# Kernel optimization log

Hardware: AMD Instinct MI355X
Metric: run time of the kernel (lower is better)

Reference implementation:

```python
import jax, jax.numpy as jnp
import numpy as np

N = 8192          # points per cloud
IN_C = 256        # in_channels
OUT_C = 256       # out_channels
SC = IN_C // 4    # shortcut_out_channels
KNN = 32          # neighbors gathered per point
KP = 15           # kernel points (standard KPConv)
RADIUS = 0.12
EXTENT = RADIUS * 2.0 / 2.5   # radius * kp_extent / conv_radius
NEG_SLOPE = 0.1
EPS = 1e-5


def setup_inputs() -> dict:
    key = jax.random.key(0)
    ks = jax.random.split(key, 10)
    src = jax.random.normal(ks[0], (N, IN_C), jnp.float32)
    tgt = jax.random.normal(ks[1], (N, IN_C), jnp.float32)
    src_coords = jax.random.uniform(ks[2], (N, 3), jnp.float32)
    tgt_coords = jax.random.uniform(ks[3], (N, 3), jnp.float32)
    W_in = jax.random.normal(ks[4], (IN_C, SC), jnp.float32) / np.sqrt(IN_C)
    b_in = jnp.zeros((SC,), jnp.float32)
    kernel_pts = jax.random.normal(ks[5], (KP, 3), jnp.float32) * (0.7 * EXTENT)
    W_kp = jax.random.normal(ks[6], (KP, SC, SC), jnp.float32) / np.sqrt(KP * SC)
    W_out = jax.random.normal(ks[7], (SC, OUT_C), jnp.float32) / np.sqrt(SC)
    b_out = jnp.zeros((OUT_C,), jnp.float32)
    gamma = jnp.ones((OUT_C,), jnp.float32)
    beta = jnp.zeros((OUT_C,), jnp.float32)
    return dict(src=src, tgt=tgt, src_coords=src_coords, tgt_coords=tgt_coords,
                W_in=W_in, b_in=b_in, kernel_pts=kernel_pts, W_kp=W_kp,
                W_out=W_out, b_out=b_out, gamma=gamma, beta=beta)


def _one_cloud(x, coords, W_in, b_in, kernel_pts, W_kp, W_out, b_out, gamma, beta):
    # 1x1 conv in: [N, IN_C] -> [N, SC]
    h = x @ W_in + b_in

    # neighbor search: kNN by squared distance, masked to the conv radius
    d2 = jnp.sum((coords[:, None, :] - coords[None, :, :]) ** 2, axis=-1)  # [N, N]
    _, idx = jax.lax.top_k(-d2, KNN)                                       # [N, KNN]
    nb_coords = coords[idx]                                                # [N, KNN, 3]
    rel = nb_coords - coords[:, None, :]                                   # [N, KNN, 3]
    in_range = jnp.sum(rel ** 2, axis=-1) <= RADIUS ** 2                   # [N, KNN]

    # KPConv: linear correlation to kernel points, masked neighbor aggregate
    diff = rel[:, :, None, :] - kernel_pts[None, None, :, :]               # [N, KNN, KP, 3]
    dist = jnp.sqrt(jnp.sum(diff ** 2, axis=-1))                           # [N, KNN, KP]
    infl = jnp.maximum(1.0 - dist / EXTENT, 0.0) * in_range[:, :, None]    # [N, KNN, KP]
    nb_feats = h[idx]                                                      # [N, KNN, SC]
    agg = jnp.einsum('nkp,nkc->npc', infl, nb_feats)                       # [N, KP, SC]
    h = jnp.einsum('npc,pcd->nd', agg, W_kp)                               # [N, SC]

    # 1x1 conv out: [N, SC] -> [N, OUT_C]
    y = h @ W_out + b_out

    # batch norm over points (training-mode statistics) + affine
    mu = jnp.mean(y, axis=0)
    var = jnp.mean((y - mu) ** 2, axis=0)
    y = gamma * (y - mu) * jax.lax.rsqrt(var + EPS) + beta

    # leaky relu
    return jnp.where(y > 0, y, NEG_SLOPE * y)


def reference(src, tgt, src_coords, tgt_coords, W_in, b_in, kernel_pts, W_kp,
              W_out, b_out, gamma, beta):
    params = (W_in, b_in, kernel_pts, W_kp, W_out, b_out, gamma, beta)
    s = _one_cloud(src, src_coords, *params)
    t = _one_cloud(tgt, tgt_coords, *params)
    return (s, t, src_coords, tgt_coords)
```

## Files before the change

### kernel.cpp

```cpp
#include <hip/hip_runtime.h>
#include <stdint.h>

#define NPTS 8192
#define KNN 32
#define KPN 15
#define SCC 64
#define OUTC 256
#define R2F 0.0144f
#define INV_EXT (1.0f/0.096f)
#define SCAP 128
#define NT 8
#define COB 32
#define GD 8
#define NCELL (GD*GD*GD)
#define KJ (KPN*SCC)
#define AGP 968

typedef float  f32x4  __attribute__((ext_vector_type(4)));
typedef __bf16 bf16x8 __attribute__((ext_vector_type(8)));
typedef __bf16 bf16x4 __attribute__((ext_vector_type(4)));

__device__ __forceinline__ int cell_of(float x) {
  int c = (int)(x * (float)GD);
  return c < 0 ? 0 : (c > GD-1 ? GD-1 : c);
}

__global__ __launch_bounds__(256) void prep_k(
    const float* __restrict__ scd, const float* __restrict__ tcd,
    float* __restrict__ out,
    const float* __restrict__ Wkp, __bf16* __restrict__ WkpT,
    const float* __restrict__ Win, __bf16* __restrict__ WinF)
{
  int b = blockIdx.x, t = threadIdx.x;
  if (b < 192) {
    int i = b*256 + t;
    out[i] = (i < NPTS*3) ? scd[i] : tcd[i - NPTS*3];
  } else if (b < 432) {
    int i = (b - 192)*256 + t;
    int j = i >> 6, d = i & 63;
    WkpT[(size_t)d*KJ + j] = (__bf16)Wkp[i];
  } else {
    int i = (b - 432)*256 + t;
    int j = i & 7, lane = (i >> 3) & 63, cc = i >> 9;
    int kc = cc >> 2, ct = cc & 3;
    int g16 = lane >> 4, p = lane & 15;
    int k = kc*32 + g16*8 + j;
    WinF[i] = (__bf16)Win[(size_t)k*64 + ct*16 + p];
  }
}

__global__ __launch_bounds__(1024) void grid_build(
    const float* __restrict__ cA, const float* __restrict__ cB,
    unsigned int* __restrict__ starts,
    unsigned int* __restrict__ cursor,
    float* __restrict__ stats)
{
  __shared__ unsigned int hcnt[2][NCELL];
  __shared__ unsigned int a[NCELL], b[NCELL];
  int t = threadIdx.x;
  if (t < NCELL) { hcnt[0][t] = 0u; hcnt[1][t] = 0u; }
  stats[t] = 0.f;
  __syncthreads();
  for (int i = t; i < 2*NPTS; i += 1024) {
    int cloud = i >> 13, n = i & 8191;
    const float* coords = cloud ? cB : cA;
    int cx = cell_of(coords[(size_t)n*3]);
    int cy = cell_of(coords[(size_t)n*3+1]);
    int cz = cell_of(coords[(size_t)n*3+2]);
    atomicAdd(&hcnt[cloud][(cz*GD + cy)*GD + cx], 1u);
  }
  __syncthreads();
  for (int cloud = 0; cloud < 2; ++cloud) {
    if (t < NCELL) a[t] = hcnt[cloud][t];
    __syncthreads();
    unsigned int *s = a, *d = b;
    for (int off = 1; off < NCELL; off <<= 1) {
      if (t < NCELL) {
        unsigned int x = s[t];
        if (t >= off) x += s[t - off];
        d[t] = x;
      }
      __syncthreads();
      unsigned int* tmp = s; s = d; d = tmp;
    }
    if (t < NCELL) {
      unsigned int inc = s[t];
      unsigned int exc = inc - hcnt[cloud][t];
      starts[cloud*520 + t] = exc;
      cursor[cloud*NCELL + t] = exc;
      if (t == NCELL-1) starts[cloud*520 + NCELL] = inc;
    }
    __syncthreads();
  }
}

__global__ __launch_bounds__(256) void grid_scatter(
    const float* __restrict__ cA, const float* __restrict__ cB,
    unsigned int* __restrict__ cursor, float4* __restrict__ sorted,
    float4* __restrict__ coords4)
{
  int i = blockIdx.x*256 + threadIdx.x;
  int cloud = i >> 13, n = i & 8191;
  const float* coords = cloud ? cB : cA;
  float x = coords[(size_t)n*3], y = coords[(size_t)n*3+1], z = coords[(size_t)n*3+2];
  coords4[(size_t)cloud*NPTS + n] = make_float4(x, y, z, 0.f);
  int cell = (cell_of(z)*GD + cell_of(y))*GD + cell_of(x);
  unsigned int slot = atomicAdd(&cursor[cloud*NCELL + cell], 1u);
  sorted[(size_t)cloud*NPTS + slot] = make_float4(x, y, z, __int_as_float(n));
}

__global__ __launch_bounds__(256) void knn_convin_k(
    const float4* __restrict__ coords4,
    const unsigned int* __restrict__ starts, const float4* __restrict__ sorted,
    short* __restrict__ fidx,
    const float* __restrict__ src, const float* __restrict__ tgt,
    const __bf16* __restrict__ WinF, const float* __restrict__ bin,
    __bf16* __restrict__ h)
{
  __shared__ unsigned long long surv[4][SCAP];
  int bId = blockIdx.x;
  int t = threadIdx.x, w = t >> 6, lane = t & 63;
  if (bId < 256) {
    int rt = bId*4 + w;
    int row0 = rt*16;
    const float* x = (row0 >> 13) ? tgt : src;
    int n0 = row0 & 8191;
    int g16 = lane >> 4, p = lane & 15;
    const float* xrow = x + (size_t)(n0 + p)*256;
    f32x4 acc[4];
    #pragma unroll
    for (int ct = 0; ct < 4; ++ct) {
      float bb = bin[ct*16 + p];
      acc[ct] = (f32x4){bb, bb, bb, bb};
    }
    #pragma unroll
    for (int kc = 0; kc < 8; ++kc) {
      float4 xa = *(const float4*)(xrow + kc*32 + g16*8);
      float4 xb = *(const float4*)(xrow + kc*32 + g16*8 + 4);
      bf16x8 af;
      af[0]=(__bf16)xa.x; af[1]=(__bf16)xa.y; af[2]=(__bf16)xa.z; af[3]=(__bf16)xa.w;
      af[4]=(__bf16)xb.x; af[5]=(__bf16)xb.y; af[6]=(__bf16)xb.z; af[7]=(__bf16)xb.w;
      #pragma unroll
      for (int ct = 0; ct < 4; ++ct) {
        bf16x8 bf = *(const bf16x8*)(WinF + (size_t)(kc*4 + ct)*512 + lane*8);
        acc[ct] = __builtin_amdgcn_mfma_f32_16x16x32_bf16(af, bf, acc[ct], 0,0,0);
      }
    }
    #pragma unroll
    for (int r = 0; r < 4; ++r) {
      bf16x4 o;
      o[0] = (__bf16)acc[0][r]; o[1] = (__bf16)acc[1][r];
      o[2] = (__bf16)acc[2][r]; o[3] = (__bf16)acc[3][r];
      *(bf16x4*)(h + (size_t)(row0 + g16*4 + r)*SCC + p*4) = o;
    }
    return;
  }
  int q = (bId - 256)*4 + w;
  int cloud = q >> 13, n = q & 8191;
  float4 qc = coords4[(size_t)cloud*NPTS + n];
  float qx = qc.x, qy = qc.y, qz = qc.z;
  int cx = cell_of(qx), cy = cell_of(qy), cz = cell_of(qz);
  const unsigned int* st = starts + cloud*520;
  const float4* sp = sorted + (size_t)cloud*NPTS;
  int c0 = cx > 0 ? cx-1 : 0;
  int c1 = cx < GD-1 ? cx+1 : GD-1;
  unsigned int cnt = 0;
  for (int dz = -1; dz <= 1; ++dz) {
    int zz = cz + dz; if (zz < 0 || zz > GD-1) continue;
    for (int dy = -1; dy <= 1; ++dy) {
      int yy = cy + dy; if (yy < 0 || yy > GD-1) continue;
      int rb = (zz*GD + yy)*GD;
      unsigned int s = st[rb + c0];
      unsigned int e = st[rb + c1 + 1];
      for (unsigned int jj = s; jj < e; jj += 64) {
        unsigned int j = jj + lane;
        bool keep = false; float d2 = 0.f; unsigned int oi = 0;
        if (j < e) {
          float4 p4 = sp[j];
          float dx = qx-p4.x, dyy = qy-p4.y, dzz = qz-p4.z;
          d2 = fmaf(dx, dx, fmaf(dyy, dyy, dzz*dzz));
          oi = __float_as_uint(p4.w);
          keep = (d2 <= R2F);
        }
        unsigned long long m = __ballot(keep);
        if (keep) {
          unsigned int before = __builtin_amdgcn_mbcnt_hi(
              (unsigned int)(m >> 32),
              __builtin_amdgcn_mbcnt_lo((unsigned int)m, 0u));
          unsigned int pos = cnt + before;
          if (pos < SCAP)
            surv[w][pos] = ((unsigned long long)__float_as_uint(d2) << 32) | oi;
        }
        cnt += (unsigned int)__popcll(m);
      }
    }
  }
  int C = (int)cnt; if (C > SCAP) C = SCAP;
  unsigned long long k0 = (lane      < C) ? surv[w][lane]      : ~0ULL;
  unsigned long long k1 = (lane + 64 < C) ? surv[w][lane + 64] : ~0ULL;
  int r0 = 0, r1 = 0;
  for (int j = 0; j < C; ++j) {
    unsigned long long kj = surv[w][j];
    r0 += (kj < k0);
    r1 += (kj < k1);
  }
  size_t g = (size_t)cloud*NPTS + n;
  if (k0 != ~0ULL && r0 < KNN) fidx[g*KNN + r0] = (short)(k0 & 0xffffu);
  if (k1 != ~0ULL && r1 < KNN) fidx[g*KNN + r1] = (short)(k1 & 0xffffu);
  if (lane >= C && lane < KNN) fidx[g*KNN + lane] = (short)-1;
}

__global__ __launch_bounds__(512) void kpconv_fused(
    const float4* __restrict__ coords4,
    const float* __restrict__ kpts, const short* __restrict__ fidx,
    const __bf16* __restrict__ h, const __bf16* __restrict__ WkpT,
    float* __restrict__ h2)
{
  __shared__ __bf16 agg_s[NT][AGP];
  __shared__ float  red2[2*4*16*17];
  int t = threadIdx.x;
  int w = t >> 6, lane = t & 63;
  int gq = blockIdx.x*NT + w;
  int cloud = gq >> 13, n = gq & 8191;
  const float4* c4 = coords4 + (size_t)cloud*NPTS;
  int idxreg = fidx[(size_t)gq*KNN + (lane & 31)];
  float4 qc = c4[n];
  float qx = qc.x, qy = qc.y, qz = qc.z;
  int g16 = lane >> 4;
  int p   = lane & 15;
  int pc  = p < KPN ? p : 0;
  float kpx = kpts[pc*3], kpy = kpts[pc*3+1], kpz = kpts[pc*3+2];
  bf16x8 afrag;
  int idxs[8];
  #pragma unroll
  for (int j = 0; j < 8; ++j) {
    int k = g16*8 + j;
    int idx = __shfl(idxreg, k);
    idxs[j] = idx < 0 ? 0 : idx;
    float4 nc = c4[idxs[j]];
    float wv = 0.f;
    if (idx >= 0 && p < KPN) {
      float dx = (nc.x - qx) - kpx;
      float dy = (nc.y - qy) - kpy;
      float dz = (nc.z - qz) - kpz;
      float d = sqrtf(fmaf(dx, dx, fmaf(dy, dy, dz*dz)));
      wv = fmaxf(1.0f - d*INV_EXT, 0.0f);
    }
    afrag[j] = (__bf16)wv;
  }
  bf16x8 bfrag0, bfrag1, bfrag2, bfrag3;
  #pragma unroll
  for (int j = 0; j < 8; ++j) {
    bf16x4 hv = *(const bf16x4*)(h + ((size_t)(cloud*NPTS + idxs[j]))*SCC + p*4);
    bfrag0[j] = hv[0];
    bfrag1[j] = hv[1];
    bfrag2[j] = hv[2];
    bfrag3[j] = hv[3];
  }
  f32x4 acc0 = {0.f,0.f,0.f,0.f}, acc1 = acc0, acc2 = acc0, acc3 = acc0;
  acc0 = __builtin_amdgcn_mfma_f32_16x16x32_bf16(afrag, bfrag0, acc0, 0, 0, 0);
  acc1 = __builtin_amdgcn_mfma_f32_16x16x32_bf16(afrag, bfrag1, acc1, 0, 0, 0);
  acc2 = __builtin_amdgcn_mfma_f32_16x16x32_bf16(afrag, bfrag2, acc2, 0, 0, 0);
  acc3 = __builtin_amdgcn_mfma_f32_16x16x32_bf16(afrag, bfrag3, acc3, 0, 0, 0);
  #pragma unroll
  for (int r = 0; r < 4; ++r) {
    int pp = g16*4 + r;
    if (pp < KPN) {
      agg_s[w][pp*SCC +      p] = (__bf16)acc0[r];
      agg_s[w][pp*SCC + 16 + p] = (__bf16)acc1[r];
      agg_s[w][pp*SCC + 32 + p] = (__bf16)acc2[r];
      agg_s[w][pp*SCC + 48 + p] = (__bf16)acc3[r];
    }
  }
  __syncthreads();
  {
    int dt = w & 3, kh = w >> 2;
    int ptb = p & 7;
    const __bf16* arow = WkpT + (size_t)(dt*16 + p)*KJ + kh*480 + g16*8;
    const __bf16* brow = &agg_s[ptb][kh*480 + g16*8];
    f32x4 accB = {0.f,0.f,0.f,0.f};
    #pragma unroll
    for (int s = 0; s < 15; ++s) {
      bf16x8 af = *(const bf16x8*)(arow + s*32);
      bf16x8 bfr = *(const bf16x8*)(brow + s*32);
      accB = __builtin_amdgcn_mfma_f32_16x16x32_bf16(af, bfr, accB, 0, 0, 0);
    }
    if (p < 8) {
      #pragma unroll
      for (int r = 0; r < 4; ++r)
        red2[((kh*4 + dt)*16 + g16*4 + r)*17 + p] = accB[r];
    }
  }
  __syncthreads();
  {
    int pt = t >> 6, d = t & 63;
    float v = red2[d*17 + pt] + red2[(64 + d)*17 + pt];
    h2[((size_t)blockIdx.x*NT + pt)*SCC + d] = v;
  }
}

__global__ __launch_bounds__(512) void conv_out_bn(
    const float* __restrict__ h2, const float* __restrict__ W,
    const float* __restrict__ b, float* __restrict__ y,
    float* __restrict__ stats)
{
  __shared__ float w_s[SCC*OUTC];
  __shared__ float h_s[COB][SCC];
  __shared__ float rs_s[2][OUTC];
  __shared__ float rs2_s[2][OUTC];
  int t = threadIdx.x;
  int d = t & 255, rg = t >> 8;
  int row0 = blockIdx.x*COB;
  int cloud = (int)(blockIdx.x >> 8);
  {
    const float4* gw = (const float4*)W;
    float4* lw = (float4*)w_s;
    #pragma unroll
    for (int i = 0; i < 8; ++i) lw[t + 512*i] = gw[t + 512*i];
    const float4* gh = (const float4*)(h2 + (size_t)row0*SCC);
    ((float4*)h_s)[t] = gh[t];
  }
  __syncthreads();
  float acc[16];
  float bb = b[d];
  #pragma unroll
  for (int r = 0; r < 16; ++r) acc[r] = bb;
  int rb = rg*16;
  #pragma unroll 4
  for (int c4 = 0; c4 < 16; ++c4) {
    float w0 = w_s[(c4*4+0)*OUTC + d];
    float w1 = w_s[(c4*4+1)*OUTC + d];
    float w2 = w_s[(c4*4+2)*OUTC + d];
    float w3 = w_s[(c4*4+3)*OUTC + d];
    #pragma unroll
    for (int r = 0; r < 16; ++r) {
      float4 hv = *(const float4*)&h_s[rb + r][c4*4];
      acc[r] = fmaf(hv.x,w0, fmaf(hv.y,w1, fmaf(hv.z,w2, fmaf(hv.w,w3, acc[r]))));
    }
  }
  float s = 0.f, s2 = 0.f;
  #pragma unroll
  for (int r = 0; r < 16; ++r) {
    float v = acc[r];
    y[((size_t)row0 + rb + r)*OUTC + d] = v;
    s += v; s2 = fmaf(v, v, s2);
  }
  rs_s[rg][d] = s; rs2_s[rg][d] = s2;
  __syncthreads();
  if (rg == 0) {
    atomicAdd(&stats[cloud*512 + d],       s  + rs_s[1][d]);
    atomicAdd(&stats[cloud*512 + 256 + d], s2 + rs2_s[1][d]);
  }
}

__global__ __launch_bounds__(256) void bn_apply_k(
    float* __restrict__ y, const float* __restrict__ stats,
    const float* __restrict__ gamma, const float* __restrict__ beta)
{
  size_t e = (size_t)blockIdx.x*256 + threadIdx.x;
  int c = (int)(e & 255);
  int cloud = (int)(e >> 21);
  float s  = stats[cloud*512 + c];
  float s2 = stats[cloud*512 + 256 + c];
  float mu  = s * (1.0f/NPTS);
  float var = fmaxf(s2 * (1.0f/NPTS) - mu*mu, 0.f);
  float sc = gamma[c] * rsqrtf(var + 1e-5f);
  float sh = beta[c] - mu*sc;
  float v = fmaf(y[e], sc, sh);
  v = v > 0.f ? v : 0.1f*v;
  y[e] = v;
}

extern "C" void kernel_launch(void* const* d_in, const int* in_sizes, int n_in,
                              void* d_out, int out_size, void* d_ws, size_t ws_size,
                              hipStream_t stream)
{
  (void)in_sizes; (void)n_in; (void)out_size; (void)ws_size;
  const float* src   = (const float*)d_in[0];
  const float* tgt   = (const float*)d_in[1];
  const float* scd   = (const float*)d_in[2];
  const float* tcd   = (const float*)d_in[3];
  const float* W_in  = (const float*)d_in[4];
  const float* b_in  = (const float*)d_in[5];
  const float* kpts  = (const float*)d_in[6];
  const float* W_kp  = (const float*)d_in[7];
  const float* W_out = (const float*)d_in[8];
  const float* b_out = (const float*)d_in[9];
  const float* gamma = (const float*)d_in[10];
  const float* beta  = (const float*)d_in[11];

  char* ws = (char*)d_ws;
  __bf16* h    = (__bf16*)ws;
  float* h2    = (float*)(ws + (4u<<20));
  short* fidx  = (short*)(ws + (8u<<20));
  float* stats = (float*)(ws + (9u<<20));
  __bf16* WkpT = (__bf16*)(ws + (9u<<20) + (64u<<10));
  __bf16* WinF = (__bf16*)(ws + (9u<<20) + (256u<<10));
  float4* coords4 = (float4*)(ws + (9u<<20) + (512u<<10));
  unsigned int* starts = (unsigned int*)(ws + (4u<<20) + (8u<<10));
  unsigned int* cursor = (unsigned int*)(ws + (4u<<20) + (16u<<10));
  float4* sorted       = (float4*)(ws + (4u<<20) + (32u<<10));

  float* yout = (float*)d_out;

  prep_k<<<496, 256, 0, stream>>>(scd, tcd, yout + (size_t)2*NPTS*OUTC,
                                  W_kp, WkpT, W_in, WinF);
  grid_build<<<1, 1024, 0, stream>>>(scd, tcd, starts, cursor, stats);
  grid_scatter<<<64, 256, 0, stream>>>(scd, tcd, cursor, sorted, coords4);
  knn_convin_k<<<4352, 256, 0, stream>>>(coords4, starts, sorted, fidx,
                                         src, tgt, WinF, b_in, h);
  kpconv_fused<<<2048, 512, 0, stream>>>(coords4, kpts, fidx, h, WkpT, h2);
  conv_out_bn<<<512, 512, 0, stream>>>(h2, W_out, b_out, yout, stats);
  bn_apply_k<<<16384, 256, 0, stream>>>(yout, stats, gamma, beta);
}
```

Before: 202.9 us.

## Process 16 spatially sorted points per block in KPConv with full-K MFMA

```diff
diff --git a/kernel.cpp b/kernel.cpp
--- a/kernel.cpp
+++ b/kernel.cpp
@@ -9,12 +9,11 @@
 #define R2F 0.0144f
 #define INV_EXT (1.0f/0.096f)
 #define SCAP 128
-#define NT 8
 #define COB 32
 #define GD 8
 #define NCELL (GD*GD*GD)
 #define KJ (KPN*SCC)
-#define AGP 968
+#define AGP2 1000
 
 typedef float  f32x4  __attribute__((ext_vector_type(4)));
 typedef __bf16 bf16x8 __attribute__((ext_vector_type(8)));
@@ -210,92 +209,102 @@
   if (lane >= C && lane < KNN) fidx[g*KNN + lane] = (short)-1;
 }
 
-__global__ __launch_bounds__(512) void kpconv_fused(
-    const float4* __restrict__ coords4,
+__global__ __launch_bounds__(512, 4) void kpconv_fused(
+    const float4* __restrict__ coords4, const float4* __restrict__ sorted,
     const float* __restrict__ kpts, const short* __restrict__ fidx,
     const __bf16* __restrict__ h, const __bf16* __restrict__ WkpT,
     float* __restrict__ h2)
 {
-  __shared__ __bf16 agg_s[NT][AGP];
-  __shared__ float  red2[2*4*16*17];
+  __shared__ __bf16 agg_s[16][AGP2];
+  __shared__ float  red2[4*16*17];
+  __shared__ int    oidx_s[16];
   int t = threadIdx.x;
   int w = t >> 6, lane = t & 63;
-  int gq = blockIdx.x*NT + w;
-  int cloud = gq >> 13, n = gq & 8191;
+  int b = blockIdx.x;
+  int cloud = b >> 9;
+  int sbase = (b & 511)*16;
   const float4* c4 = coords4 + (size_t)cloud*NPTS;
-  int idxreg = fidx[(size_t)gq*KNN + (lane & 31)];
-  float4 qc = c4[n];
-  float qx = qc.x, qy = qc.y, qz = qc.z;
+  const float4* sp = sorted + (size_t)cloud*NPTS;
   int g16 = lane >> 4;
   int p   = lane & 15;
   int pc  = p < KPN ? p : 0;
   float kpx = kpts[pc*3], kpy = kpts[pc*3+1], kpz = kpts[pc*3+2];
-  bf16x8 afrag;
-  int idxs[8];
+  bf16x8 afrag[2];
+  int idxs[2][8];
+  int orig[2];
   #pragma unroll
-  for (int j = 0; j < 8; ++j) {
-    int k = g16*8 + j;
-    int idx = __shfl(idxreg, k);
-    idxs[j] = idx < 0 ? 0 : idx;
-    float4 nc = c4[idxs[j]];
-    float wv = 0.f;
-    if (idx >= 0 && p < KPN) {
-      float dx = (nc.x - qx) - kpx;
-      float dy = (nc.y - qy) - kpy;
-      float dz = (nc.z - qz) - kpz;
-      float d = sqrtf(fmaf(dx, dx, fmaf(dy, dy, dz*dz)));
-      wv = fmaxf(1.0f - d*INV_EXT, 0.0f);
-    }
-    afrag[j] = (__bf16)wv;
-  }
-  bf16x8 bfrag0, bfrag1, bfrag2, bfrag3;
+  for (int hf = 0; hf < 2; ++hf) {
+    int lp = w*2 + hf;
+    float4 se = sp[sbase + lp];
+    int o = (int)__float_as_uint(se.w);
+    orig[hf] = o;
+    if (lane == 0) oidx_s[lp] = o;
+    int idxreg = fidx[((size_t)cloud*NPTS + o)*KNN + (lane & 31)];
+    float qx = se.x, qy = se.y, qz = se.z;
+    #pragma unroll
+    for (int j = 0; j < 8; ++j) {
+      int k = g16*8 + j;
+      int idx = __shfl(idxreg, k);
+      idxs[hf][j] = idx < 0 ? 0 : idx;
+      float4 nc = c4[idxs[hf][j]];
+      float wv = 0.f;
+      if (idx >= 0 && p < KPN) {
+        float dx = (nc.x - qx) - kpx;
+        float dy = (nc.y - qy) - kpy;
+        float dz = (nc.z - qz) - kpz;
+        float d = sqrtf(fmaf(dx, dx, fmaf(dy, dy, dz*dz)));
+        wv = fmaxf(1.0f - d*INV_EXT, 0.0f);
+      }
+      afrag[hf][j] = (__bf16)wv;
+    }
+  }
   #pragma unroll
-  for (int j = 0; j < 8; ++j) {
-    bf16x4 hv = *(const bf16x4*)(h + ((size_t)(cloud*NPTS + idxs[j]))*SCC + p*4);
-    bfrag0[j] = hv[0];
-    bfrag1[j] = hv[1];
-    bfrag2[j] = hv[2];
-    bfrag3[j] = hv[3];
-  }
-  f32x4 acc0 = {0.f,0.f,0.f,0.f}, acc1 = acc0, acc2 = acc0, acc3 = acc0;
-  acc0 = __builtin_amdgcn_mfma_f32_16x16x32_bf16(afrag, bfrag0, acc0, 0, 0, 0);
-  acc1 = __builtin_amdgcn_mfma_f32_16x16x32_bf16(afrag, bfrag1, acc1, 0, 0, 0);
-  acc2 = __builtin_amdgcn_mfma_f32_16x16x32_bf16(afrag, bfrag2, acc2, 0, 0, 0);
-  acc3 = __builtin_amdgcn_mfma_f32_16x16x32_bf16(afrag, bfrag3, acc3, 0, 0, 0);
-  #pragma unroll
-  for (int r = 0; r < 4; ++r) {
-    int pp = g16*4 + r;
-    if (pp < KPN) {
-      agg_s[w][pp*SCC +      p] = (__bf16)acc0[r];
-      agg_s[w][pp*SCC + 16 + p] = (__bf16)acc1[r];
-      agg_s[w][pp*SCC + 32 + p] = (__bf16)acc2[r];
-      agg_s[w][pp*SCC + 48 + p] = (__bf16)acc3[r];
-    }
-  }
-  __syncthreads();
-  {
-    int dt = w & 3, kh = w >> 2;
-    int ptb = p & 7;
-    const __bf16* arow = WkpT + (size_t)(dt*16 + p)*KJ + kh*480 + g16*8;
-    const __bf16* brow = &agg_s[ptb][kh*480 + g16*8];
+  for (int hf = 0; hf < 2; ++hf) {
+    bf16x8 bfrag0, bfrag1, bfrag2, bfrag3;
+    #pragma unroll
+    for (int j = 0; j < 8; ++j) {
+      bf16x4 hv = *(const bf16x4*)(h + ((size_t)cloud*NPTS + idxs[hf][j])*SCC + p*4);
+      bfrag0[j] = hv[0]; bfrag1[j] = hv[1]; bfrag2[j] = hv[2]; bfrag3[j] = hv[3];
+    }
+    f32x4 a0 = {0.f,0.f,0.f,0.f}, a1 = a0, a2 = a0, a3 = a0;
+    a0 = __builtin_amdgcn_mfma_f32_16x16x32_bf16(afrag[hf], bfrag0, a0, 0,0,0);
+    a1 = __builtin_amdgcn_mfma_f32_16x16x32_bf16(afrag[hf], bfrag1, a1, 0,0,0);
+    a2 = __builtin_amdgcn_mfma_f32_16x16x32_bf16(afrag[hf], bfrag2, a2, 0,0,0);
+    a3 = __builtin_amdgcn_mfma_f32_16x16x32_bf16(afrag[hf], bfrag3, a3, 0,0,0);
+    int lp = w*2 + hf;
+    #pragma unroll
+    for (int r = 0; r < 4; ++r) {
+      int pp = g16*4 + r;
+      if (pp < KPN) {
+        agg_s[lp][pp*SCC +      p] = (__bf16)a0[r];
+        agg_s[lp][pp*SCC + 16 + p] = (__bf16)a1[r];
+        agg_s[lp][pp*SCC + 32 + p] = (__bf16)a2[r];
+        agg_s[lp][pp*SCC + 48 + p] = (__bf16)a3[r];
+      }
+    }
+  }
+  __syncthreads();
+  if (w < 4) {
+    int dt = w;
+    const __bf16* arow = WkpT + (size_t)(dt*16 + p)*KJ + g16*8;
+    const __bf16* brow = &agg_s[p][g16*8];
     f32x4 accB = {0.f,0.f,0.f,0.f};
     #pragma unroll
-    for (int s = 0; s < 15; ++s) {
-      bf16x8 af = *(const bf16x8*)(arow + s*32);
+    for (int s = 0; s < 30; ++s) {
+      bf16x8 af  = *(const bf16x8*)(arow + s*32);
       bf16x8 bfr = *(const bf16x8*)(brow + s*32);
       accB = __builtin_amdgcn_mfma_f32_16x16x32_bf16(af, bfr, accB, 0, 0, 0);
     }
-    if (p < 8) {
-      #pragma unroll
-      for (int r = 0; r < 4; ++r)
-        red2[((kh*4 + dt)*16 + g16*4 + r)*17 + p] = accB[r];
-    }
-  }
-  __syncthreads();
-  {
-    int pt = t >> 6, d = t & 63;
-    float v = red2[d*17 + pt] + red2[(64 + d)*17 + pt];
-    h2[((size_t)blockIdx.x*NT + pt)*SCC + d] = v;
+    #pragma unroll
+    for (int r = 0; r < 4; ++r)
+      red2[(dt*16 + g16*4 + r)*17 + p] = accB[r];
+  }
+  __syncthreads();
+  #pragma unroll
+  for (int e = t; e < 1024; e += 512) {
+    int pt = e >> 6, d = e & 63;
+    float v = red2[((d >> 4)*16 + (d & 15))*17 + pt];
+    h2[((size_t)cloud*NPTS + oidx_s[pt])*SCC + d] = v;
   }
 }
 
@@ -397,9 +406,9 @@
   __bf16* WkpT = (__bf16*)(ws + (9u<<20) + (64u<<10));
   __bf16* WinF = (__bf16*)(ws + (9u<<20) + (256u<<10));
   float4* coords4 = (float4*)(ws + (9u<<20) + (512u<<10));
-  unsigned int* starts = (unsigned int*)(ws + (4u<<20) + (8u<<10));
-  unsigned int* cursor = (unsigned int*)(ws + (4u<<20) + (16u<<10));
-  float4* sorted       = (float4*)(ws + (4u<<20) + (32u<<10));
+  float4* sorted  = (float4*)(ws + (10u<<20));
+  unsigned int* starts = (unsigned int*)(ws + (10u<<20) + (512u<<10));
+  unsigned int* cursor = (unsigned int*)(ws + (10u<<20) + (520u<<10));
 
   float* yout = (float*)d_out;
 
@@ -409,7 +418,7 @@
   grid_scatter<<<64, 256, 0, stream>>>(scd, tcd, cursor, sorted, coords4);
   knn_convin_k<<<4352, 256, 0, stream>>>(coords4, starts, sorted, fidx,
                                          src, tgt, WinF, b_in, h);
-  kpconv_fused<<<2048, 512, 0, stream>>>(coords4, kpts, fidx, h, WkpT, h2);
+  kpconv_fused<<<1024, 512, 0, stream>>>(coords4, sorted, kpts, fidx, h, WkpT, h2);
   conv_out_bn<<<512, 512, 0, stream>>>(h2, W_out, b_out, yout, stats);
   bn_apply_k<<<16384, 256, 0, stream>>>(yout, stats, gamma, beta);
 }
```

Measured after the change: 195.9 us. -3.5%, faster.
